# Kernel optimization log

Hardware: AMD Instinct MI355X
Metric: run time of the kernel (lower is better)

The kernel has to match this reference:

```python
import jax, jax.numpy as jnp
import numpy as np

N_NODES = 100000
N_EDGES = 1600000
N_CLASS = 10
HIDDEN = 128
BN_EPS = 1e-5


def _bn(h, gamma, beta):
    # BatchNorm1d in training mode: biased batch statistics over the node dim
    m = h.mean(axis=0)
    v = ((h - m) ** 2).mean(axis=0)
    return gamma * (h - m) / jnp.sqrt(v + BN_EPS) + beta


def _mlp(h, w1, b1, g1, t1, w2, b2, g2, t2):
    h = jax.nn.relu(_bn(h @ w1 + b1, g1, t1))
    h = jax.nn.relu(_bn(h @ w2 + b2, g2, t2))
    return h


def _gin_conv(x, edge_index, mlp_params):
    src, dst = edge_index[0], edge_index[1]
    # sum-aggregate neighbor messages: [E, D] gather + scatter-add -> [N, D]
    agg = jax.ops.segment_sum(x[src], dst, num_segments=N_NODES)
    h = x + agg  # (1 + eps) * x + agg, eps = 0
    return _mlp(h, *mlp_params)


def setup_inputs() -> dict:
    key = jax.random.key(0)
    ks = jax.random.split(key, 16)
    x = jax.random.normal(ks[0], (N_NODES, N_CLASS), dtype=jnp.float32)
    edge_index = jax.random.randint(ks[1], (2, N_EDGES), 0, N_NODES, dtype=jnp.int64)
    edge_weight = jax.random.uniform(ks[2], (N_EDGES,), dtype=jnp.float32)

    def lin(k, fan_in, fan_out):
        bound = 1.0 / np.sqrt(fan_in)
        kw, kb = jax.random.split(k)
        w = jax.random.uniform(kw, (fan_in, fan_out), minval=-bound, maxval=bound, dtype=jnp.float32)
        b = jax.random.uniform(kb, (fan_out,), minval=-bound, maxval=bound, dtype=jnp.float32)
        return w, b

    w11, b11 = lin(ks[3], N_CLASS, HIDDEN)
    w12, b12 = lin(ks[4], HIDDEN, HIDDEN)
    w21, b21 = lin(ks[5], HIDDEN, HIDDEN)
    w22, b22 = lin(ks[6], HIDDEN, HIDDEN)
    wf, bf = lin(ks[7], HIDDEN, N_CLASS)
    ones = jnp.ones((HIDDEN,), jnp.float32)
    zeros = jnp.zeros((HIDDEN,), jnp.float32)
    return {
        "x": x, "edge_weight": edge_weight,
        "w11": w11, "b11": b11, "g11": ones, "t11": zeros,
        "w12": w12, "b12": b12, "g12": ones, "t12": zeros,
        "w21": w21, "b21": b21, "g21": ones, "t21": zeros,
        "w22": w22, "b22": b22, "g22": ones, "t22": zeros,
        "wf": wf, "bf": bf,
        "edge_index": edge_index,
    }


def reference(x, edge_weight, w11, b11, g11, t11, w12, b12, g12, t12,
              w21, b21, g21, t21, w22, b22, g22, t22, wf, bf, edge_index):
    h = jax.nn.relu(_gin_conv(x, edge_index, (w11, b11, g11, t11, w12, b12, g12, t12)))
    h = jax.nn.relu(_gin_conv(h, edge_index, (w21, b21, g21, t21, w22, b22, g22, t22)))
    logits = h @ wf + bf
    return jax.nn.log_softmax(logits, axis=1)
```

## Files before the change

### kernel.cpp

```cpp
#include <hip/hip_runtime.h>
#include <hip/hip_bf16.h>

#define N_CLASS 10
#define HIDDEN 128
#define BN_EPS 1e-5f

typedef short short8 __attribute__((ext_vector_type(8)));
typedef float floatx4 __attribute__((ext_vector_type(4)));

__device__ __forceinline__ float bf2f(unsigned short u) {
    unsigned int x = ((unsigned int)u) << 16;
    float f; __builtin_memcpy(&f, &x, 4); return f;
}
__device__ __forceinline__ unsigned short f2bf(float f) {
    unsigned int x; __builtin_memcpy(&x, &f, 4);
    x += 0x7FFFu + ((x >> 16) & 1u);
    return (unsigned short)(x >> 16);
}
__device__ __forceinline__ unsigned int pack2bf(float a, float b) {
    __hip_bfloat162 h = __float22bfloat162_rn(make_float2(a, b));
    unsigned int u; __builtin_memcpy(&u, &h, 4); return u;
}
__device__ __forceinline__ float lo_f(unsigned int u) {
    unsigned int x = u << 16; float f; __builtin_memcpy(&f, &x, 4); return f;
}
__device__ __forceinline__ float hi_f(unsigned int u) {
    unsigned int x = u & 0xffff0000u; float f; __builtin_memcpy(&f, &x, 4); return f;
}

__global__ __launch_bounds__(512) void bhist_k(const int* __restrict__ ei,
                                               int* __restrict__ bhist,
                                               int* __restrict__ bbase, int E) {
    __shared__ int h[512];
    int tid = threadIdx.x;
    h[tid] = 0;
    __syncthreads();
    int chunk = (E + gridDim.x - 1) / gridDim.x;
    int e0 = blockIdx.x * chunk;
    int e1 = min(e0 + chunk, E);
    for (int e = e0 + tid; e < e1; e += 512)
        atomicAdd(&h[((unsigned)ei[E + e]) >> 8], 1);
    __syncthreads();
    bbase[tid * 256 + blockIdx.x] = h[tid];
    if (h[tid]) atomicAdd(&bhist[tid], h[tid]);
}

__global__ __launch_bounds__(512) void bscan_k(const int* __restrict__ bhist,
                                               int* __restrict__ bstart, int NBK) {
    __shared__ int sm[512];
    int t = threadIdx.x;
    sm[t] = (t < NBK) ? bhist[t] : 0;
    __syncthreads();
    for (int off = 1; off < 512; off <<= 1) {
        int u = (t >= off) ? sm[t - off] : 0;
        __syncthreads();
        sm[t] += u;
        __syncthreads();
    }
    bstart[t] = (t == 0) ? 0 : sm[t - 1];
    if (t == 0) bstart[512] = sm[511];
}

__global__ __launch_bounds__(256) void bscan2_k(int* __restrict__ bbase,
                                                const int* __restrict__ bstart) {
    __shared__ int sm[256];
    int b = blockIdx.x;
    int t = threadIdx.x;
    int v = bbase[b * 256 + t];
    sm[t] = v;
    __syncthreads();
    for (int off = 1; off < 256; off <<= 1) {
        int u = (t >= off) ? sm[t - off] : 0;
        __syncthreads();
        sm[t] += u;
        __syncthreads();
    }
    bbase[b * 256 + t] = bstart[b] + sm[t] - v;
}

__global__ __launch_bounds__(512) void bscatter_k(const int* __restrict__ ei,
                                                  const int* __restrict__ bbase,
                                                  unsigned int* __restrict__ pairs, int E) {
    __shared__ int base[512], cur[512];
    int tid = threadIdx.x;
    base[tid] = bbase[tid * 256 + blockIdx.x];
    cur[tid] = 0;
    __syncthreads();
    int chunk = (E + gridDim.x - 1) / gridDim.x;
    int e0 = blockIdx.x * chunk;
    int e1 = min(e0 + chunk, E);
    for (int e = e0 + tid; e < e1; e += 512) {
        unsigned int s = (unsigned int)ei[e];
        unsigned int d = (unsigned int)ei[E + e];
        int bk = d >> 8;
        int r = atomicAdd(&cur[bk], 1);
        pairs[base[bk] + r] = s | ((d & 255u) << 24);
    }
}

__global__ __launch_bounds__(512) void bcsr_k(const unsigned int* __restrict__ pairs,
                                              const int* __restrict__ bstart,
                                              int* __restrict__ row_ptr,
                                              int* __restrict__ cnt,
                                              int* __restrict__ col, int N) {
    __shared__ int h[256], sc[256], cur[256];
    int tid = threadIdx.x;
    if (tid < 256) { h[tid] = 0; cur[tid] = 0; }
    __syncthreads();
    int b = blockIdx.x, lo = b << 8;
    int s = bstart[b], e = bstart[b + 1];
    for (int i = s + tid; i < e; i += 512)
        atomicAdd(&h[pairs[i] >> 24], 1);
    __syncthreads();
    if (tid < 256) sc[tid] = h[tid];
    __syncthreads();
    for (int off = 1; off < 256; off <<= 1) {
        int u = (tid < 256 && tid >= off) ? sc[tid - off] : 0;
        __syncthreads();
        if (tid < 256) sc[tid] += u;
        __syncthreads();
    }
    if (tid < 256) {
        int d = lo + tid;
        if (d < N) { cnt[d] = h[tid]; row_ptr[d] = s + sc[tid] - h[tid]; }
        sc[tid] -= h[tid];
    }
    __syncthreads();
    for (int i = s + tid; i < e; i += 512) {
        unsigned int p = pairs[i];
        int d = p >> 24;
        int r = atomicAdd(&cur[d], 1);
        col[s + sc[d] + r] = (int)(p & 0xFFFFFFu);
    }
}

__global__ void prep_k(const float* __restrict__ W0, const float* __restrict__ W1,
                       const float* __restrict__ W2,
                       unsigned short* __restrict__ T0, unsigned short* __restrict__ T1,
                       unsigned short* __restrict__ T2,
                       float* __restrict__ stats, int* __restrict__ bhist) {
    int y = blockIdx.y;
    int i = blockIdx.x * 256 + threadIdx.x;
    const float* W = (y == 0) ? W0 : (y == 1) ? W1 : W2;
    unsigned short* T = (y == 0) ? T0 : (y == 1) ? T1 : T2;
    if (i < 128 * 128) {
        int k = i >> 7, n = i & 127;
        T[n * 128 + k] = f2bf(W[k * 128 + n]);
    }
    if (y == 0) {
        if (i < 1024) stats[i] = 0.f;
        if (i < 512)  bhist[i] = 0;
    }
}

__global__ void padx_k(const float* __restrict__ X, unsigned short* __restrict__ XP, int N) {
    int i = blockIdx.x * 256 + threadIdx.x;
    if (i >= N * 16) return;
    int node = i >> 4, f = i & 15;
    XP[i] = (f < N_CLASS) ? f2bf(X[node * N_CLASS + f]) : (unsigned short)0;
}

__global__ void gather10_k(const unsigned short* __restrict__ XP, const int* __restrict__ col,
                           const int* __restrict__ rp, const int* __restrict__ cnt,
                           float* __restrict__ out, int N) {
    int t = blockIdx.x * 256 + threadIdx.x;
    int node = t >> 4, f = t & 15;
    if (node >= N) return;
    int start = rp[node], deg = cnt[node];
    float acc = bf2f(XP[node * 16 + f]);
    int j = 0;
    for (; j + 8 <= deg; j += 8) {
        int s0 = col[start + j],     s1 = col[start + j + 1];
        int s2 = col[start + j + 2], s3 = col[start + j + 3];
        int s4 = col[start + j + 4], s5 = col[start + j + 5];
        int s6 = col[start + j + 6], s7 = col[start + j + 7];
        float v0 = bf2f(XP[s0 * 16 + f]);
        float v1 = bf2f(XP[s1 * 16 + f]);
        float v2 = bf2f(XP[s2 * 16 + f]);
        float v3 = bf2f(XP[s3 * 16 + f]);
        float v4 = bf2f(XP[s4 * 16 + f]);
        float v5 = bf2f(XP[s5 * 16 + f]);
        float v6 = bf2f(XP[s6 * 16 + f]);
        float v7 = bf2f(XP[s7 * 16 + f]);
        acc += v0; acc += v1; acc += v2; acc += v3;
        acc += v4; acc += v5; acc += v6; acc += v7;
    }
    for (; j < deg; ++j)
        acc += bf2f(XP[col[start + j] * 16 + f]);
    out[node * 16 + f] = acc;
}

__global__ __launch_bounds__(256) void act2_k(
    const unsigned short* __restrict__ Z, unsigned short* __restrict__ R,
    const float* __restrict__ st, const float* __restrict__ g,
    const float* __restrict__ b, int N, float inv_n) {
    __shared__ float sTab[128], hTab[128];
    int tid = threadIdx.x;
    if (tid < 128) {
        float m = st[tid] * inv_n;
        float v = fmaxf(st[128 + tid] * inv_n - m * m, 0.f);
        float s = g[tid] * rsqrtf(v + BN_EPS);
        sTab[tid] = s;
        hTab[tid] = b[tid] - m * s;
    }
    __syncthreads();
    int total = N * 16;
    for (int i = blockIdx.x * 256 + tid; i < total; i += gridDim.x * 256) {
        int k8 = (i & 15) * 8;
        uint4 v = ((const uint4*)Z)[i];
        unsigned int* uw = (unsigned int*)&v;
#pragma unroll
        for (int j = 0; j < 4; ++j) {
            int kb = k8 + j * 2;
            float f0 = fmaxf(fmaf(lo_f(uw[j]), sTab[kb],     hTab[kb]),     0.f);
            float f1 = fmaxf(fmaf(hi_f(uw[j]), sTab[kb + 1], hTab[kb + 1]), 0.f);
            uw[j] = pack2bf(f0, f1);
        }
        ((uint4*)R)[i] = v;
    }
}

__global__ __launch_bounds__(256) void gather_sum_k(
    const unsigned short* __restrict__ R, const int* __restrict__ col,
    const int* __restrict__ rp, const int* __restrict__ cnt,
    unsigned short* __restrict__ out, int N) {
    int wave = __builtin_amdgcn_readfirstlane((blockIdx.x * 256 + threadIdx.x) >> 6);
    int lane = threadIdx.x & 63;
    if (wave >= N) return;
    int start = __builtin_amdgcn_readfirstlane(rp[wave]);
    int deg   = __builtin_amdgcn_readfirstlane(cnt[wave]);
    const unsigned int* Xv = (const unsigned int*)R;
    unsigned int self = Xv[wave * 64 + lane];
    float a0 = lo_f(self);
    float a1 = hi_f(self);
    int j = 0;
    for (; j + 16 <= deg; j += 16) {
        int n0  = col[start + j],      n1  = col[start + j + 1];
        int n2  = col[start + j + 2],  n3  = col[start + j + 3];
        int n4  = col[start + j + 4],  n5  = col[start + j + 5];
        int n6  = col[start + j + 6],  n7  = col[start + j + 7];
        int n8  = col[start + j + 8],  n9  = col[start + j + 9];
        int n10 = col[start + j + 10], n11 = col[start + j + 11];
        int n12 = col[start + j + 12], n13 = col[start + j + 13];
        int n14 = col[start + j + 14], n15 = col[start + j + 15];
        unsigned int w0  = Xv[n0  * 64 + lane];
        unsigned int w1  = Xv[n1  * 64 + lane];
        unsigned int w2  = Xv[n2  * 64 + lane];
        unsigned int w3  = Xv[n3  * 64 + lane];
        unsigned int w4  = Xv[n4  * 64 + lane];
        unsigned int w5  = Xv[n5  * 64 + lane];
        unsigned int w6  = Xv[n6  * 64 + lane];
        unsigned int w7  = Xv[n7  * 64 + lane];
        unsigned int w8  = Xv[n8  * 64 + lane];
        unsigned int w9  = Xv[n9  * 64 + lane];
        unsigned int w10 = Xv[n10 * 64 + lane];
        unsigned int w11 = Xv[n11 * 64 + lane];
        unsigned int w12 = Xv[n12 * 64 + lane];
        unsigned int w13 = Xv[n13 * 64 + lane];
        unsigned int w14 = Xv[n14 * 64 + lane];
        unsigned int w15 = Xv[n15 * 64 + lane];
        a0 += lo_f(w0);  a1 += hi_f(w0);
        a0 += lo_f(w1);  a1 += hi_f(w1);
        a0 += lo_f(w2);  a1 += hi_f(w2);
        a0 += lo_f(w3);  a1 += hi_f(w3);
        a0 += lo_f(w4);  a1 += hi_f(w4);
        a0 += lo_f(w5);  a1 += hi_f(w5);
        a0 += lo_f(w6);  a1 += hi_f(w6);
        a0 += lo_f(w7);  a1 += hi_f(w7);
        a0 += lo_f(w8);  a1 += hi_f(w8);
        a0 += lo_f(w9);  a1 += hi_f(w9);
        a0 += lo_f(w10); a1 += hi_f(w10);
        a0 += lo_f(w11); a1 += hi_f(w11);
        a0 += lo_f(w12); a1 += hi_f(w12);
        a0 += lo_f(w13); a1 += hi_f(w13);
        a0 += lo_f(w14); a1 += hi_f(w14);
        a0 += lo_f(w15); a1 += hi_f(w15);
    }
    for (; j + 8 <= deg; j += 8) {
        int n0 = col[start + j],     n1 = col[start + j + 1];
        int n2 = col[start + j + 2], n3 = col[start + j + 3];
        int n4 = col[start + j + 4], n5 = col[start + j + 5];
        int n6 = col[start + j + 6], n7 = col[start + j + 7];
        unsigned int w0 = Xv[n0 * 64 + lane];
        unsigned int w1 = Xv[n1 * 64 + lane];
        unsigned int w2 = Xv[n2 * 64 + lane];
        unsigned int w3 = Xv[n3 * 64 + lane];
        unsigned int w4 = Xv[n4 * 64 + lane];
        unsigned int w5 = Xv[n5 * 64 + lane];
        unsigned int w6 = Xv[n6 * 64 + lane];
        unsigned int w7 = Xv[n7 * 64 + lane];
        a0 += lo_f(w0); a1 += hi_f(w0);
        a0 += lo_f(w1); a1 += hi_f(w1);
        a0 += lo_f(w2); a1 += hi_f(w2);
        a0 += lo_f(w3); a1 += hi_f(w3);
        a0 += lo_f(w4); a1 += hi_f(w4);
        a0 += lo_f(w5); a1 += hi_f(w5);
        a0 += lo_f(w6); a1 += hi_f(w6);
        a0 += lo_f(w7); a1 += hi_f(w7);
    }
    for (; j < deg; ++j) {
        unsigned int v = Xv[col[start + j] * 64 + lane];
        a0 += lo_f(v); a1 += hi_f(v);
    }
    ((unsigned int*)out)[wave * 64 + lane] = pack2bf(a0, a1);
}

__global__ __launch_bounds__(128) void gemm10_k(
    const float* __restrict__ A, const float* __restrict__ W,
    const float* __restrict__ bias, unsigned short* __restrict__ C,
    float* __restrict__ stOut, int N) {
    __shared__ float rb[16 * 16];
    const int tid = threadIdx.x;
    float wreg[N_CLASS];
#pragma unroll
    for (int k = 0; k < N_CLASS; ++k) wreg[k] = W[k * HIDDEN + tid];
    float bb = bias[tid];
    float s = 0.f, s2 = 0.f;
    for (int r0 = blockIdx.x * 16; r0 < N; r0 += gridDim.x * 16) {
        int nr = min(16, N - r0);
        for (int i = tid; i < nr * 16; i += 128) rb[i] = A[r0 * 16 + i];
        __syncthreads();
        for (int r = 0; r < nr; ++r) {
            float acc = bb;
#pragma unroll
            for (int k = 0; k < N_CLASS; ++k) acc = fmaf(rb[r * 16 + k], wreg[k], acc);
            C[(r0 + r) * HIDDEN + tid] = f2bf(acc);
            s += acc; s2 += acc * acc;
        }
        __syncthreads();
    }
    atomicAdd(stOut + tid, s);
    atomicAdd(stOut + HIDDEN + tid, s2);
}

template<bool BN>
__global__ __launch_bounds__(256, 3) void gemm_mfma_k(
    const unsigned short* __restrict__ Zin, const unsigned short* __restrict__ Wt,
    const float* __restrict__ bias,
    const float* __restrict__ stIn, const float* __restrict__ gIn,
    const float* __restrict__ tIn,
    unsigned short* __restrict__ Zout, float* __restrict__ stOut,
    int N, float inv_n) {
    __shared__ unsigned short Wl[128 * 136];
    __shared__ unsigned short Al[64 * 136];
    __shared__ float sTab[128], hTab[128], biasTab[128];

    const int tid  = threadIdx.x;
    const int wv   = tid >> 6;
    const int ln   = tid & 63;
    const int half = ln >> 4;
    const int l16  = ln & 15;

    if (tid < 128) {
        biasTab[tid] = bias[tid];
        if (BN) {
            float m = stIn[tid] * inv_n;
            float v = fmaxf(stIn[128 + tid] * inv_n - m * m, 0.f);
            float s = gIn[tid] * rsqrtf(v + BN_EPS);
            sTab[tid] = s;
            hTab[tid] = tIn[tid] - m * s;
        }
    }
    for (int c = tid; c < 2048; c += 256) {
        int n = c >> 4, k8 = c & 15;
        uint4 v = *(const uint4*)(Wt + n * 128 + k8 * 8);
        *(uint4*)(&Wl[n * 136 + k8 * 8]) = v;
    }
    __syncthreads();

    float cs[8], cs2[8];
#pragma unroll
    for (int i = 0; i < 8; ++i) { cs[i] = 0.f; cs2[i] = 0.f; }

    const int ntiles = (N + 63) >> 6;
    for (int tile = blockIdx.x; tile < ntiles; tile += gridDim.x) {
        const int r0 = tile * 64;
        for (int c = tid; c < 1024; c += 256) {
            int r = c >> 4, k8 = c & 15;
            int gr = r0 + r; if (gr >= N) gr = N - 1;
            uint4 v = *(const uint4*)(Zin + gr * 128 + k8 * 8);
            if (BN) {
                unsigned int* uw = (unsigned int*)&v;
                int kb = k8 * 8;
#pragma unroll
                for (int j = 0; j < 4; ++j) {
                    int kk = kb + j * 2;
                    float f0 = fmaxf(fmaf(lo_f(uw[j]), sTab[kk],     hTab[kk]),     0.f);
                    float f1 = fmaxf(fmaf(hi_f(uw[j]), sTab[kk + 1], hTab[kk + 1]), 0.f);
                    uw[j] = pack2bf(f0, f1);
                }
            }
            *(uint4*)(&Al[r * 136 + k8 * 8]) = v;
        }
        __syncthreads();

        short8 afrag[4];
        const int arow = wv * 16 + l16;
#pragma unroll
        for (int s = 0; s < 4; ++s)
            afrag[s] = *(const short8*)(&Al[arow * 136 + s * 32 + half * 8]);
        __syncthreads();

#pragma unroll
        for (int ct = 0; ct < 8; ++ct) {
            floatx4 acc = {0.f, 0.f, 0.f, 0.f};
            const int bn_ = ct * 16 + l16;
#pragma unroll
            for (int s = 0; s < 4; ++s) {
                short8 bfrag = *(const short8*)(&Wl[bn_ * 136 + s * 32 + half * 8]);
                acc = __builtin_amdgcn_mfma_f32_16x16x32_bf16(afrag[s], bfrag, acc, 0, 0, 0);
            }
            float bcol = biasTab[bn_];
#pragma unroll
            for (int r = 0; r < 4; ++r) {
                int lrow = wv * 16 + half * 4 + r;
                float val = acc[r] + bcol;
                if (r0 + lrow < N) { cs[ct] += val; cs2[ct] += val * val; }
                Al[lrow * 136 + bn_] = f2bf(val);
            }
        }
        __syncthreads();

        for (int c = tid; c < 1024; c += 256) {
            int r = c >> 4, k8 = c & 15;
            int gr = r0 + r;
            if (gr < N)
                *(uint4*)(Zout + gr * 128 + k8 * 8) = *(const uint4*)(&Al[r * 136 + k8 * 8]);
        }
        __syncthreads();
    }

    float* red = (float*)Al;
    if (tid < 256) red[tid] = 0.f;
    __syncthreads();
#pragma unroll
    for (int ct = 0; ct < 8; ++ct) {
        float a = cs[ct], b = cs2[ct];
        a += __shfl_xor(a, 16); a += __shfl_xor(a, 32);
        b += __shfl_xor(b, 16); b += __shfl_xor(b, 32);
        if (half == 0) {
            atomicAdd(&red[ct * 16 + l16], a);
            atomicAdd(&red[128 + ct * 16 + l16], b);
        }
    }
    __syncthreads();
    if (tid < 128) {
        atomicAdd(stOut + tid, red[tid]);
        atomicAdd(stOut + 128 + tid, red[128 + tid]);
    }
}

__global__ __launch_bounds__(256) void final_mfma_k(
    const unsigned short* __restrict__ Z, const float* __restrict__ st,
    const float* __restrict__ g, const float* __restrict__ b,
    const float* __restrict__ wf, const float* __restrict__ bfc,
    float* __restrict__ out, int N, float inv_n) {
    __shared__ unsigned short Al[64 * 136];
    __shared__ unsigned short Bl[16 * 136];
    __shared__ float sTab[128], hTab[128], biasTab[16];

    const int tid  = threadIdx.x;
    const int wv   = tid >> 6;
    const int ln   = tid & 63;
    const int half = ln >> 4;
    const int l16  = ln & 15;

    if (tid < 128) {
        float m = st[tid] * inv_n;
        float v = fmaxf(st[128 + tid] * inv_n - m * m, 0.f);
        float s = g[tid] * rsqrtf(v + BN_EPS);
        sTab[tid] = s;
        hTab[tid] = b[tid] - m * s;
    }
    if (tid < 16) biasTab[tid] = (tid < N_CLASS) ? bfc[tid] : -3.0e38f;
    {
        int n = tid >> 4, k8 = (tid & 15) * 8;
        uint4 v;
        unsigned short* us = (unsigned short*)&v;
#pragma unroll
        for (int j = 0; j < 8; ++j)
            us[j] = (n < N_CLASS) ? f2bf(wf[(k8 + j) * N_CLASS + n]) : (unsigned short)0;
        *(uint4*)(&Bl[n * 136 + k8]) = v;
    }
    __syncthreads();

    short8 bfrag[4];
#pragma unroll
    for (int s = 0; s < 4; ++s)
        bfrag[s] = *(const short8*)(&Bl[l16 * 136 + s * 32 + half * 8]);

    const int ntiles = (N + 63) >> 6;
    for (int tile = blockIdx.x; tile < ntiles; tile += gridDim.x) {
        const int r0 = tile * 64;
        for (int c = tid; c < 1024; c += 256) {
            int r = c >> 4, k8 = c & 15;
            int gr = r0 + r; if (gr >= N) gr = N - 1;
            uint4 v = *(const uint4*)(Z + gr * 128 + k8 * 8);
            unsigned int* uw = (unsigned int*)&v;
            int kb = k8 * 8;
#pragma unroll
            for (int j = 0; j < 4; ++j) {
                int kk = kb + j * 2;
                float f0 = fmaxf(fmaf(lo_f(uw[j]), sTab[kk],     hTab[kk]),     0.f);
                float f1 = fmaxf(fmaf(hi_f(uw[j]), sTab[kk + 1], hTab[kk + 1]), 0.f);
                uw[j] = pack2bf(f0, f1);
            }
            *(uint4*)(&Al[r * 136 + k8 * 8]) = v;
        }
        __syncthreads();

        short8 afrag[4];
        const int arow = wv * 16 + l16;
#pragma unroll
        for (int s = 0; s < 4; ++s)
            afrag[s] = *(const short8*)(&Al[arow * 136 + s * 32 + half * 8]);
        __syncthreads();

        floatx4 acc = {0.f, 0.f, 0.f, 0.f};
#pragma unroll
        for (int s = 0; s < 4; ++s)
            acc = __builtin_amdgcn_mfma_f32_16x16x32_bf16(afrag[s], bfrag[s], acc, 0, 0, 0);

        float bcol = biasTab[l16];
#pragma unroll
        for (int r = 0; r < 4; ++r) {
            float lg = acc[r] + bcol;
            float mx = lg;
            mx = fmaxf(mx, __shfl_xor(mx, 1));
            mx = fmaxf(mx, __shfl_xor(mx, 2));
            mx = fmaxf(mx, __shfl_xor(mx, 4));
            mx = fmaxf(mx, __shfl_xor(mx, 8));
            float p = __expf(lg - mx);
            float se = p;
            se += __shfl_xor(se, 1);
            se += __shfl_xor(se, 2);
            se += __shfl_xor(se, 4);
            se += __shfl_xor(se, 8);
            float ls = __logf(se);
            int grow = r0 + wv * 16 + half * 4 + r;
            if (l16 < N_CLASS && grow < N)
                out[grow * N_CLASS + l16] = lg - mx - ls;
        }
    }
}


extern "C" void kernel_launch(void* const* d_in, const int* in_sizes, int n_in,
                              void* d_out, int out_size, void* d_ws, size_t ws_size,
                              hipStream_t stream) {
    const float* x   = (const float*)d_in[0];
    const float* w11 = (const float*)d_in[2];
    const float* b11 = (const float*)d_in[3];
    const float* g11 = (const float*)d_in[4];
    const float* t11 = (const float*)d_in[5];
    const float* w12 = (const float*)d_in[6];
    const float* b12 = (const float*)d_in[7];
    const float* g12 = (const float*)d_in[8];
    const float* t12 = (const float*)d_in[9];
    const float* w21 = (const float*)d_in[10];
    const float* b21 = (const float*)d_in[11];
    const float* g21 = (const float*)d_in[12];
    const float* t21 = (const float*)d_in[13];
    const float* w22 = (const float*)d_in[14];
    const float* b22 = (const float*)d_in[15];
    const float* g22 = (const float*)d_in[16];
    const float* t22 = (const float*)d_in[17];
    const float* wf  = (const float*)d_in[18];
    const float* bf  = (const float*)d_in[19];
    const int*   ei  = (const int*)d_in[20];

    const int N = in_sizes[0] / N_CLASS;
    const int E = in_sizes[1];
    const float inv_n = 1.0f / (float)N;
    const int NBK = (N + 255) >> 8;

    char* base = (char*)d_ws;
    size_t off = 0;
    auto take = [&](size_t bytes) { void* p = base + off; off += (bytes + 255) & ~(size_t)255; return p; };
    float*          stats   = (float*)take(1024 * 4);
    unsigned short* xp      = (unsigned short*)take((size_t)N * 16 * 2);
    float*          h0      = (float*)take((size_t)N * 16 * 4);
    int*            cnt     = (int*)take((size_t)N * 4);
    int*            row_ptr = (int*)take((size_t)N * 4);
    int*            bhist   = (int*)take(512 * 4);
    int*            bstart  = (int*)take(520 * 4);
    int*            bbase   = (int*)take(512 * 256 * 4);
    unsigned int*   pairs   = (unsigned int*)take((size_t)E * 4);
    int*            col     = (int*)take((size_t)E * 4);
    unsigned short* bufA    = (unsigned short*)take((size_t)N * HIDDEN * 2);
    unsigned short* bufB    = (unsigned short*)take((size_t)N * HIDDEN * 2);
    unsigned short* bufC    = (unsigned short*)take((size_t)N * HIDDEN * 2);
    unsigned short* Wt1     = (unsigned short*)take(128 * 128 * 2);
    unsigned short* Wt2     = (unsigned short*)take(128 * 128 * 2);
    unsigned short* Wt3     = (unsigned short*)take(128 * 128 * 2);

    prep_k<<<dim3(64, 3), 256, 0, stream>>>(w12, w21, w22, Wt1, Wt2, Wt3,
                                            stats, bhist);
    padx_k<<<(N * 16 + 255) / 256, 256, 0, stream>>>(x, xp, N);

    bhist_k<<<256, 512, 0, stream>>>(ei, bhist, bbase, E);
    bscan_k<<<1, 512, 0, stream>>>(bhist, bstart, NBK);
    bscan2_k<<<NBK, 256, 0, stream>>>(bbase, bstart);
    bscatter_k<<<256, 512, 0, stream>>>(ei, bbase, pairs, E);
    bcsr_k<<<NBK, 512, 0, stream>>>(pairs, bstart, row_ptr, cnt, col, N);

    gather10_k<<<(N * 16 + 255) / 256, 256, 0, stream>>>(xp, col, row_ptr, cnt, h0, N);
    gemm10_k<<<512, 128, 0, stream>>>(h0, w11, b11, bufA, stats, N);
    gemm_mfma_k<true><<<768, 256, 0, stream>>>(bufA, Wt1, b12, stats, g11, t11,
                                               bufB, stats + 256, N, inv_n);

    act2_k<<<3125, 256, 0, stream>>>(bufB, bufC, stats + 256, g12, t12, N, inv_n);
    gather_sum_k<<<(N * 64 + 255) / 256, 256, 0, stream>>>(bufC, col, row_ptr, cnt,
                                                           bufA, N);

    gemm_mfma_k<false><<<768, 256, 0, stream>>>(bufA, Wt2, b21, nullptr, nullptr, nullptr,
                                                bufB, stats + 512, N, inv_n);
    gemm_mfma_k<true><<<768, 256, 0, stream>>>(bufB, Wt3, b22, stats + 512, g21, t21,
                                               bufA, stats + 768, N, inv_n);

    final_mfma_k<<<782, 256, 0, stream>>>(bufA, stats + 768, g22, t22,
                                          wf, bf, (float*)d_out, N, inv_n);
}
```

Before: 378.4 us.

## Load MFMA A-fragments directly from global per wave, drop LDS staging

The GEMM and final kernels now have each wave own a 16-row tile and load its A fragments straight from global memory into registers, removing the shared-memory A buffer and the block-wide barriers around it. GEMM outputs are written directly to global as scattered 2-byte stores instead of being staged in LDS and written as coalesced 16-byte rows. This cuts LDS use and synchronization but risks less efficient global stores, and the launch bound, grid size and occupancy hint are also changed.

```diff
diff --git a/kernel.cpp b/kernel.cpp
--- a/kernel.cpp
+++ b/kernel.cpp
@@ -334,7 +334,7 @@
 }
 
 template<bool BN>
-__global__ __launch_bounds__(256, 3) void gemm_mfma_k(
+__global__ __launch_bounds__(256) void gemm_mfma_k(
     const unsigned short* __restrict__ Zin, const unsigned short* __restrict__ Wt,
     const float* __restrict__ bias,
     const float* __restrict__ stIn, const float* __restrict__ gIn,
@@ -342,11 +342,10 @@
     unsigned short* __restrict__ Zout, float* __restrict__ stOut,
     int N, float inv_n) {
     __shared__ unsigned short Wl[128 * 136];
-    __shared__ unsigned short Al[64 * 136];
     __shared__ float sTab[128], hTab[128], biasTab[128];
+    __shared__ float red[256];
 
     const int tid  = threadIdx.x;
-    const int wv   = tid >> 6;
     const int ln   = tid & 63;
     const int half = ln >> 4;
     const int l16  = ln & 15;
@@ -361,6 +360,7 @@
             hTab[tid] = tIn[tid] - m * s;
         }
     }
+    red[tid] = 0.f;
     for (int c = tid; c < 2048; c += 256) {
         int n = c >> 4, k8 = c & 15;
         uint4 v = *(const uint4*)(Wt + n * 128 + k8 * 8);
@@ -372,16 +372,20 @@
 #pragma unroll
     for (int i = 0; i < 8; ++i) { cs[i] = 0.f; cs2[i] = 0.f; }
 
-    const int ntiles = (N + 63) >> 6;
-    for (int tile = blockIdx.x; tile < ntiles; tile += gridDim.x) {
-        const int r0 = tile * 64;
-        for (int c = tid; c < 1024; c += 256) {
-            int r = c >> 4, k8 = c & 15;
-            int gr = r0 + r; if (gr >= N) gr = N - 1;
-            uint4 v = *(const uint4*)(Zin + gr * 128 + k8 * 8);
+    const int ntiles = (N + 15) >> 4;
+    const int gw = (blockIdx.x << 2) | (tid >> 6);
+    const int nw = gridDim.x << 2;
+
+    for (int t = gw; t < ntiles; t += nw) {
+        const int r0 = t << 4;
+        int arow = r0 + l16; if (arow >= N) arow = N - 1;
+        short8 afrag[4];
+#pragma unroll
+        for (int s = 0; s < 4; ++s) {
+            uint4 v = *(const uint4*)(Zin + arow * 128 + s * 32 + half * 8);
             if (BN) {
                 unsigned int* uw = (unsigned int*)&v;
-                int kb = k8 * 8;
+                int kb = s * 32 + half * 8;
 #pragma unroll
                 for (int j = 0; j < 4; ++j) {
                     int kk = kb + j * 2;
@@ -390,16 +394,8 @@
                     uw[j] = pack2bf(f0, f1);
                 }
             }
-            *(uint4*)(&Al[r * 136 + k8 * 8]) = v;
-        }
-        __syncthreads();
-
-        short8 afrag[4];
-        const int arow = wv * 16 + l16;
-#pragma unroll
-        for (int s = 0; s < 4; ++s)
-            afrag[s] = *(const short8*)(&Al[arow * 136 + s * 32 + half * 8]);
-        __syncthreads();
+            __builtin_memcpy(&afrag[s], &v, 16);
+        }
 
 #pragma unroll
         for (int ct = 0; ct < 8; ++ct) {
@@ -413,26 +409,16 @@
             float bcol = biasTab[bn_];
 #pragma unroll
             for (int r = 0; r < 4; ++r) {
-                int lrow = wv * 16 + half * 4 + r;
+                int grow = r0 + half * 4 + r;
                 float val = acc[r] + bcol;
-                if (r0 + lrow < N) { cs[ct] += val; cs2[ct] += val * val; }
-                Al[lrow * 136 + bn_] = f2bf(val);
+                if (grow < N) {
+                    cs[ct] += val; cs2[ct] += val * val;
+                    Zout[grow * 128 + bn_] = f2bf(val);
+                }
             }
         }
-        __syncthreads();
-
-        for (int c = tid; c < 1024; c += 256) {
-            int r = c >> 4, k8 = c & 15;
-            int gr = r0 + r;
-            if (gr < N)
-                *(uint4*)(Zout + gr * 128 + k8 * 8) = *(const uint4*)(&Al[r * 136 + k8 * 8]);
-        }
-        __syncthreads();
-    }
-
-    float* red = (float*)Al;
-    if (tid < 256) red[tid] = 0.f;
-    __syncthreads();
+    }
+
 #pragma unroll
     for (int ct = 0; ct < 8; ++ct) {
         float a = cs[ct], b = cs2[ct];
@@ -455,12 +441,10 @@
     const float* __restrict__ g, const float* __restrict__ b,
     const float* __restrict__ wf, const float* __restrict__ bfc,
     float* __restrict__ out, int N, float inv_n) {
-    __shared__ unsigned short Al[64 * 136];
     __shared__ unsigned short Bl[16 * 136];
     __shared__ float sTab[128], hTab[128], biasTab[16];
 
     const int tid  = threadIdx.x;
-    const int wv   = tid >> 6;
     const int ln   = tid & 63;
     const int half = ln >> 4;
     const int l16  = ln & 15;
@@ -489,15 +473,19 @@
     for (int s = 0; s < 4; ++s)
         bfrag[s] = *(const short8*)(&Bl[l16 * 136 + s * 32 + half * 8]);
 
-    const int ntiles = (N + 63) >> 6;
-    for (int tile = blockIdx.x; tile < ntiles; tile += gridDim.x) {
-        const int r0 = tile * 64;
-        for (int c = tid; c < 1024; c += 256) {
-            int r = c >> 4, k8 = c & 15;
-            int gr = r0 + r; if (gr >= N) gr = N - 1;
-            uint4 v = *(const uint4*)(Z + gr * 128 + k8 * 8);
+    const int ntiles = (N + 15) >> 4;
+    const int gw = (blockIdx.x << 2) | (tid >> 6);
+    const int nw = gridDim.x << 2;
+
+    for (int t = gw; t < ntiles; t += nw) {
+        const int r0 = t << 4;
+        int arow = r0 + l16; if (arow >= N) arow = N - 1;
+        short8 afrag[4];
+#pragma unroll
+        for (int s = 0; s < 4; ++s) {
+            uint4 v = *(const uint4*)(Z + arow * 128 + s * 32 + half * 8);
             unsigned int* uw = (unsigned int*)&v;
-            int kb = k8 * 8;
+            int kb = s * 32 + half * 8;
 #pragma unroll
             for (int j = 0; j < 4; ++j) {
                 int kk = kb + j * 2;
@@ -505,16 +493,8 @@
                 float f1 = fmaxf(fmaf(hi_f(uw[j]), sTab[kk + 1], hTab[kk + 1]), 0.f);
                 uw[j] = pack2bf(f0, f1);
             }
-            *(uint4*)(&Al[r * 136 + k8 * 8]) = v;
-        }
-        __syncthreads();
-
-        short8 afrag[4];
-        const int arow = wv * 16 + l16;
-#pragma unroll
-        for (int s = 0; s < 4; ++s)
-            afrag[s] = *(const short8*)(&Al[arow * 136 + s * 32 + half * 8]);
-        __syncthreads();
+            __builtin_memcpy(&afrag[s], &v, 16);
+        }
 
         floatx4 acc = {0.f, 0.f, 0.f, 0.f};
 #pragma unroll
@@ -537,7 +517,7 @@
             se += __shfl_xor(se, 4);
             se += __shfl_xor(se, 8);
             float ls = __logf(se);
-            int grow = r0 + wv * 16 + half * 4 + r;
+            int grow = r0 + half * 4 + r;
             if (l16 < N_CLASS && grow < N)
                 out[grow * N_CLASS + l16] = lg - mx - ls;
         }
@@ -606,16 +586,16 @@
 
     gather10_k<<<(N * 16 + 255) / 256, 256, 0, stream>>>(xp, col, row_ptr, cnt, h0, N);
     gemm10_k<<<512, 128, 0, stream>>>(h0, w11, b11, bufA, stats, N);
-    gemm_mfma_k<true><<<768, 256, 0, stream>>>(bufA, Wt1, b12, stats, g11, t11,
+    gemm_mfma_k<true><<<782, 256, 0, stream>>>(bufA, Wt1, b12, stats, g11, t11,
                                                bufB, stats + 256, N, inv_n);
 
     act2_k<<<3125, 256, 0, stream>>>(bufB, bufC, stats + 256, g12, t12, N, inv_n);
     gather_sum_k<<<(N * 64 + 255) / 256, 256, 0, stream>>>(bufC, col, row_ptr, cnt,
                                                            bufA, N);
 
-    gemm_mfma_k<false><<<768, 256, 0, stream>>>(bufA, Wt2, b21, nullptr, nullptr, nullptr,
+    gemm_mfma_k<false><<<782, 256, 0, stream>>>(bufA, Wt2, b21, nullptr, nullptr, nullptr,
                                                 bufB, stats + 512, N, inv_n);
-    gemm_mfma_k<true><<<768, 256, 0, stream>>>(bufB, Wt3, b22, stats + 512, g21, t21,
+    gemm_mfma_k<true><<<782, 256, 0, stream>>>(bufB, Wt3, b22, stats + 512, g21, t21,
                                                bufA, stats + 768, N, inv_n);
 
     final_mfma_k<<<782, 256, 0, stream>>>(bufA, stats + 768, g22, t22,
```

Measured after the change: 400.4 us. 5.8% more time.
